# Performance work log

Measured on AMD Instinct MI355X. Metric: run time of the kernel, lower is better.

Reference implementation:

```python
import jax, jax.numpy as jnp
import numpy as np


def setup_inputs() -> dict:
    key = jax.random.key(0)
    kx, kq, kb, kc = jax.random.split(key, 4)
    N, D = 16384, 1024
    x = jax.random.normal(kx, (N, D), dtype=jnp.float32)
    Q = jax.random.normal(kq, (D, D), dtype=jnp.float32)
    b = jax.random.normal(kb, (D,), dtype=jnp.float32)
    c = jax.random.normal(kc, (1,), dtype=jnp.float32)
    return {"x": x, "Q": Q, "b": b, "c": c}


def reference(x, Q, b, c):
    # y_i = x_i^T Q x_i + b^T x_i + c  (same math as diag(x @ Q @ x.T)
    # without materializing the NxN matrix)
    xQ = x @ Q                                # [N, D]
    quad = jnp.sum(xQ * x, axis=-1)           # [N]
    y = quad + x @ b + c                       # [N] (c broadcasts from [1])
    return y[:, None]                          # [N, 1]
```

## Files before the change

### kernel.cpp

```cpp
#include <hip/hip_runtime.h>
#include <hip/hip_bf16.h>


#define DD 1024
#define KH 128
#define NPH 16
#define BUF_SHORTS 4096

typedef short v8s __attribute__((ext_vector_type(8)));
typedef float v4f __attribute__((ext_vector_type(4)));

#define AS1(p) ((const __attribute__((address_space(1))) void*)(p))
#define AS3(p) ((__attribute__((address_space(3))) void*)(p))

__device__ __forceinline__ short f2b(float f) {
    union { __hip_bfloat16 h; short s; } u;
    u.h = __float2bfloat16(f);
    return u.s;
}

__global__ __launch_bounds__(256)
void convert_q(const float* __restrict__ Q, short* __restrict__ qb)
{
    const int i = blockIdx.x * 256 + threadIdx.x;
    const float4 f = ((const float4*)Q)[i];
    short4 s;
    s.x = f2b(f.x); s.y = f2b(f.y); s.z = f2b(f.z); s.w = f2b(f.w);
    ((short4*)qb)[i] = s;
}

template<bool PRE>
__device__ __forceinline__
void quad_body(const float* __restrict__ x, const float* __restrict__ Qf,
               const short* __restrict__ Qb, const float* __restrict__ bvec,
               const float* __restrict__ cptr, float* __restrict__ y)
{
    __shared__ short lq[2][BUF_SHORTS];

    const int tid  = threadIdx.x;
    const int lane = tid & 63;
    const int quad = lane >> 4;
    const int l15  = lane & 15;
    const int wave = tid >> 6;

    const int seg  = blockIdx.x & 15;
    const int rblk = blockIdx.x >> 4;
    const int kq   = seg >> 1;
    const int cs   = seg & 1;

    const int row_base = rblk * 256 + wave * 64;
    const int kofs   = kq * KH;
    const int nbase0 = cs * 512;

    int srow[2], schunk[2];
    #pragma unroll
    for (int i = 0; i < 2; ++i) {
        const int slot = i * 256 + tid;
        const int r = slot >> 4, cp = slot & 15;
        srow[i] = r;
        schunk[i] = cp ^ (r & 7);
    }

    float4 pf[4];

    if (PRE) {
        #pragma unroll
        for (int i = 0; i < 2; ++i) {
            const short* src = Qb + (size_t)(nbase0 + srow[i]) * DD + kofs + schunk[i] * 8;
            __builtin_amdgcn_global_load_lds(AS1(src), AS3(&lq[0][(i * 256 + tid) * 8]), 16, 0, 0);
        }
    } else {
        #pragma unroll
        for (int i = 0; i < 2; ++i) {
            const float* src = Qf + (size_t)(nbase0 + srow[i]) * DD + kofs + schunk[i] * 8;
            pf[i * 2 + 0] = *(const float4*)(src);
            pf[i * 2 + 1] = *(const float4*)(src + 4);
        }
    }

    v8s a[4][4];
    #pragma unroll
    for (int g = 0; g < 4; ++g) {
        const float* xr = x + (size_t)(row_base + g * 16 + l15) * DD + kofs + quad * 8;
        #pragma unroll
        for (int s = 0; s < 4; ++s) {
            const float4 f0 = *(const float4*)(xr + s * 32);
            const float4 f1 = *(const float4*)(xr + s * 32 + 4);
            v8s t;
            t[0]=f2b(f0.x); t[1]=f2b(f0.y); t[2]=f2b(f0.z); t[3]=f2b(f0.w);
            t[4]=f2b(f1.x); t[5]=f2b(f1.y); t[6]=f2b(f1.z); t[7]=f2b(f1.w);
            a[g][s] = t;
            asm volatile("" : "+a"(a[g][s]));
        }
    }

    float acc[4][4];
    #pragma unroll
    for (int g = 0; g < 4; ++g)
        #pragma unroll
        for (int r = 0; r < 4; ++r) acc[g][r] = 0.f;

    for (int p = 0; p < NPH; ++p) {
        if (!PRE) {
            #pragma unroll
            for (int i = 0; i < 2; ++i) {
                const float4 f0 = pf[i * 2 + 0];
                const float4 f1 = pf[i * 2 + 1];
                v8s t;
                t[0]=f2b(f0.x); t[1]=f2b(f0.y); t[2]=f2b(f0.z); t[3]=f2b(f0.w);
                t[4]=f2b(f1.x); t[5]=f2b(f1.y); t[6]=f2b(f1.z); t[7]=f2b(f1.w);
                *(v8s*)&lq[p & 1][(i * 256 + tid) * 8] = t;
            }
        }
        __syncthreads();

        if (p + 1 < NPH) {
            const size_t base = (size_t)(nbase0 + (p + 1) * 32) * DD + kofs;
            if (PRE) {
                #pragma unroll
                for (int i = 0; i < 2; ++i) {
                    const short* src = Qb + base + (size_t)srow[i] * DD + schunk[i] * 8;
                    __builtin_amdgcn_global_load_lds(AS1(src),
                        AS3(&lq[(p + 1) & 1][(i * 256 + tid) * 8]), 16, 0, 0);
                }
            } else {
                #pragma unroll
                for (int i = 0; i < 2; ++i) {
                    const float* src = Qf + base + (size_t)srow[i] * DD + schunk[i] * 8;
                    pf[i * 2 + 0] = *(const float4*)(src);
                    pf[i * 2 + 1] = *(const float4*)(src + 4);
                }
            }
        }

        #pragma unroll
        for (int tau = 0; tau < 2; ++tau) {
            const int n = nbase0 + p * 32 + tau * 16 + l15;
            const float bn = (kq == 0) ? bvec[n] : 0.f;

            float xv[4][4];
            {
                const float* xc = x + (size_t)(row_base + quad * 4) * DD + n;
                #pragma unroll
                for (int g = 0; g < 4; ++g)
                    #pragma unroll
                    for (int r = 0; r < 4; ++r)
                        xv[g][r] = xc[(size_t)(g * 16 + r) * DD];
            }

            v4f cf[4];
            #pragma unroll
            for (int g = 0; g < 4; ++g) cf[g] = (v4f){0.f, 0.f, 0.f, 0.f};

            #pragma unroll
            for (int s = 0; s < 4; ++s) {
                const int phys = (quad + 4 * s) ^ (l15 & 7);
                const v8s bf = *(const v8s*)&lq[p & 1][((tau * 16 + l15) << 7) + (phys << 3)];
                #pragma unroll
                for (int g = 0; g < 4; ++g)
                    cf[g] = __builtin_amdgcn_mfma_f32_16x16x32_bf16(a[g][s], bf, cf[g], 0, 0, 0);
            }

            #pragma unroll
            for (int g = 0; g < 4; ++g)
                #pragma unroll
                for (int r = 0; r < 4; ++r)
                    acc[g][r] += (cf[g][r] + bn) * xv[g][r];
        }
    }

    const float cc = (seg == 0) ? cptr[0] : 0.f;
    #pragma unroll
    for (int g = 0; g < 4; ++g) {
        #pragma unroll
        for (int r = 0; r < 4; ++r) {
            float v = acc[g][r];
            v += __shfl_xor(v, 1); v += __shfl_xor(v, 2);
            v += __shfl_xor(v, 4); v += __shfl_xor(v, 8);
            if (l15 == 0)
                atomicAdd(&y[row_base + g * 16 + quad * 4 + r], v + cc);
        }
    }
}

__global__ __launch_bounds__(256, 3)
void quad_pre(const float* __restrict__ x, const short* __restrict__ Qb,
              const float* __restrict__ bvec, const float* __restrict__ cptr,
              float* __restrict__ y)
{
    quad_body<true>(x, nullptr, Qb, bvec, cptr, y);
}

__global__ __launch_bounds__(256, 2)
void quad_fp32(const float* __restrict__ x, const float* __restrict__ Qf,
               const float* __restrict__ bvec, const float* __restrict__ cptr,
               float* __restrict__ y)
{
    quad_body<false>(x, Qf, nullptr, bvec, cptr, y);
}

extern "C" void kernel_launch(void* const* d_in, const int* in_sizes, int n_in,
                              void* d_out, int out_size, void* d_ws, size_t ws_size,
                              hipStream_t stream)
{
    const float* x = (const float*)d_in[0];
    const float* Q = (const float*)d_in[1];
    const float* b = (const float*)d_in[2];
    const float* c = (const float*)d_in[3];
    float* y = (float*)d_out;

    hipMemsetAsync(y, 0, (size_t)out_size * sizeof(float), stream);

    if (ws_size >= (size_t)DD * DD * sizeof(short)) {
        short* qb = (short*)d_ws;
        convert_q<<<dim3(1024), dim3(256), 0, stream>>>(Q, qb);
        quad_pre<<<dim3(1024), dim3(256), 0, stream>>>(x, qb, b, c, y);
    } else {
        quad_fp32<<<dim3(1024), dim3(256), 0, stream>>>(x, Q, b, c, y);
    }
}
```

Baseline: 166.8 us.

## Double K-slice depth per block, widen Q phase tiles, prefetch x columns

Each block now covers a 256-wide K slice and loads 64 Q rows per phase, which halves the number of k-segments and the grid size. Fewer segments mean each x element is re-read by fewer blocks and fewer atomic partial sums reach y. The x-column and b values for the next 16-column tile are prefetched in registers while the current MFMAs run. In exchange, register use (a[4][8] held in AGPRs) and LDS per block (64 KB) both double, occupancy drops to 2 blocks per CU, and the grid shrinks to 512 blocks.

```diff
diff --git a/kernel.cpp b/kernel.cpp
--- a/kernel.cpp
+++ b/kernel.cpp
@@ -3,9 +3,11 @@
 
 
 #define DD 1024
-#define KH 128
-#define NPH 16
-#define BUF_SHORTS 4096
+#define KH 256
+#define KSTEP 8
+#define NPH 8
+#define ROW_SH 256
+#define BUF_SH (64 * ROW_SH)
 
 typedef short v8s __attribute__((ext_vector_type(8)));
 typedef float v4f __attribute__((ext_vector_type(4)));
@@ -35,55 +37,58 @@
                const short* __restrict__ Qb, const float* __restrict__ bvec,
                const float* __restrict__ cptr, float* __restrict__ y)
 {
-    __shared__ short lq[2][BUF_SHORTS];
+    __shared__ short lq[2][BUF_SH];
 
     const int tid  = threadIdx.x;
     const int lane = tid & 63;
+    const int wave = tid >> 6;
     const int quad = lane >> 4;
     const int l15  = lane & 15;
-    const int wave = tid >> 6;
-
-    const int seg  = blockIdx.x & 15;
-    const int rblk = blockIdx.x >> 4;
+
+    const int seg  = blockIdx.x & 7;
+    const int rblk = blockIdx.x >> 3;
     const int kq   = seg >> 1;
     const int cs   = seg & 1;
 
     const int row_base = rblk * 256 + wave * 64;
-    const int kofs   = kq * KH;
-    const int nbase0 = cs * 512;
-
-    int srow[2], schunk[2];
-    #pragma unroll
-    for (int i = 0; i < 2; ++i) {
+    const int kofs  = kq * KH;
+    const int nbase = cs * 512;
+
+    int srow[8], schunk[8];
+    #pragma unroll
+    for (int i = 0; i < 8; ++i) {
         const int slot = i * 256 + tid;
-        const int r = slot >> 4, cp = slot & 15;
+        const int r = slot >> 5, cp = slot & 31;
         srow[i] = r;
         schunk[i] = cp ^ (r & 7);
     }
 
-    float4 pf[4];
-
     if (PRE) {
         #pragma unroll
-        for (int i = 0; i < 2; ++i) {
-            const short* src = Qb + (size_t)(nbase0 + srow[i]) * DD + kofs + schunk[i] * 8;
-            __builtin_amdgcn_global_load_lds(AS1(src), AS3(&lq[0][(i * 256 + tid) * 8]), 16, 0, 0);
+        for (int i = 0; i < 8; ++i) {
+            const short* src = Qb + (size_t)(nbase + srow[i]) * DD + kofs + schunk[i] * 8;
+            __builtin_amdgcn_global_load_lds(AS1(src),
+                AS3(&lq[0][(i * 256 + tid) * 8]), 16, 0, 0);
         }
     } else {
         #pragma unroll
-        for (int i = 0; i < 2; ++i) {
-            const float* src = Qf + (size_t)(nbase0 + srow[i]) * DD + kofs + schunk[i] * 8;
-            pf[i * 2 + 0] = *(const float4*)(src);
-            pf[i * 2 + 1] = *(const float4*)(src + 4);
-        }
-    }
-
-    v8s a[4][4];
+        for (int i = 0; i < 8; ++i) {
+            const float* src = Qf + (size_t)(nbase + srow[i]) * DD + kofs + schunk[i] * 8;
+            const float4 f0 = *(const float4*)(src);
+            const float4 f1 = *(const float4*)(src + 4);
+            v8s t;
+            t[0]=f2b(f0.x); t[1]=f2b(f0.y); t[2]=f2b(f0.z); t[3]=f2b(f0.w);
+            t[4]=f2b(f1.x); t[5]=f2b(f1.y); t[6]=f2b(f1.z); t[7]=f2b(f1.w);
+            *(v8s*)&lq[0][(i * 256 + tid) * 8] = t;
+        }
+    }
+
+    v8s a[4][KSTEP];
     #pragma unroll
     for (int g = 0; g < 4; ++g) {
         const float* xr = x + (size_t)(row_base + g * 16 + l15) * DD + kofs + quad * 8;
         #pragma unroll
-        for (int s = 0; s < 4; ++s) {
+        for (int s = 0; s < KSTEP; ++s) {
             const float4 f0 = *(const float4*)(xr + s * 32);
             const float4 f1 = *(const float4*)(xr + s * 32 + 4);
             v8s t;
@@ -101,51 +106,58 @@
         for (int r = 0; r < 4; ++r) acc[g][r] = 0.f;
 
     for (int p = 0; p < NPH; ++p) {
-        if (!PRE) {
-            #pragma unroll
-            for (int i = 0; i < 2; ++i) {
-                const float4 f0 = pf[i * 2 + 0];
-                const float4 f1 = pf[i * 2 + 1];
-                v8s t;
-                t[0]=f2b(f0.x); t[1]=f2b(f0.y); t[2]=f2b(f0.z); t[3]=f2b(f0.w);
-                t[4]=f2b(f1.x); t[5]=f2b(f1.y); t[6]=f2b(f1.z); t[7]=f2b(f1.w);
-                *(v8s*)&lq[p & 1][(i * 256 + tid) * 8] = t;
-            }
-        }
         __syncthreads();
 
         if (p + 1 < NPH) {
-            const size_t base = (size_t)(nbase0 + (p + 1) * 32) * DD + kofs;
+            const size_t nb = (size_t)(nbase + (p + 1) * 64) * DD + kofs;
+            short* dst = &lq[(p + 1) & 1][0];
             if (PRE) {
                 #pragma unroll
-                for (int i = 0; i < 2; ++i) {
-                    const short* src = Qb + base + (size_t)srow[i] * DD + schunk[i] * 8;
+                for (int i = 0; i < 8; ++i) {
+                    const short* src = Qb + nb + (size_t)srow[i] * DD + schunk[i] * 8;
                     __builtin_amdgcn_global_load_lds(AS1(src),
-                        AS3(&lq[(p + 1) & 1][(i * 256 + tid) * 8]), 16, 0, 0);
+                        AS3(&dst[(i * 256 + tid) * 8]), 16, 0, 0);
                 }
             } else {
                 #pragma unroll
-                for (int i = 0; i < 2; ++i) {
-                    const float* src = Qf + base + (size_t)srow[i] * DD + schunk[i] * 8;
-                    pf[i * 2 + 0] = *(const float4*)(src);
-                    pf[i * 2 + 1] = *(const float4*)(src + 4);
+                for (int i = 0; i < 8; ++i) {
+                    const float* src = Qf + nb + (size_t)srow[i] * DD + schunk[i] * 8;
+                    const float4 f0 = *(const float4*)(src);
+                    const float4 f1 = *(const float4*)(src + 4);
+                    v8s t;
+                    t[0]=f2b(f0.x); t[1]=f2b(f0.y); t[2]=f2b(f0.z); t[3]=f2b(f0.w);
+                    t[4]=f2b(f1.x); t[5]=f2b(f1.y); t[6]=f2b(f1.z); t[7]=f2b(f1.w);
+                    *(v8s*)&dst[(i * 256 + tid) * 8] = t;
                 }
             }
         }
 
-        #pragma unroll
-        for (int tau = 0; tau < 2; ++tau) {
-            const int n = nbase0 + p * 32 + tau * 16 + l15;
-            const float bn = (kq == 0) ? bvec[n] : 0.f;
-
-            float xv[4][4];
-            {
+        const short* buf = &lq[p & 1][0];
+
+        float xva[4][4], xvb[4][4];
+        float bna, bnb;
+        {
+            const int n = nbase + p * 64 + l15;
+            bna = (kq == 0) ? bvec[n] : 0.f;
+            const float* xc = x + (size_t)(row_base + quad * 4) * DD + n;
+            #pragma unroll
+            for (int g = 0; g < 4; ++g)
+                #pragma unroll
+                for (int r = 0; r < 4; ++r)
+                    xva[g][r] = xc[(size_t)(g * 16 + r) * DD];
+        }
+
+        #pragma unroll
+        for (int tau = 0; tau < 4; ++tau) {
+            if (tau < 3) {
+                const int n = nbase + p * 64 + (tau + 1) * 16 + l15;
+                bnb = (kq == 0) ? bvec[n] : 0.f;
                 const float* xc = x + (size_t)(row_base + quad * 4) * DD + n;
                 #pragma unroll
                 for (int g = 0; g < 4; ++g)
                     #pragma unroll
                     for (int r = 0; r < 4; ++r)
-                        xv[g][r] = xc[(size_t)(g * 16 + r) * DD];
+                        xvb[g][r] = xc[(size_t)(g * 16 + r) * DD];
             }
 
             v4f cf[4];
@@ -153,9 +165,9 @@
             for (int g = 0; g < 4; ++g) cf[g] = (v4f){0.f, 0.f, 0.f, 0.f};
 
             #pragma unroll
-            for (int s = 0; s < 4; ++s) {
-                const int phys = (quad + 4 * s) ^ (l15 & 7);
-                const v8s bf = *(const v8s*)&lq[p & 1][((tau * 16 + l15) << 7) + (phys << 3)];
+            for (int s = 0; s < KSTEP; ++s) {
+                const int phys = (s * 4 + quad) ^ (l15 & 7);
+                const v8s bf = *(const v8s*)&buf[(tau * 16 + l15) * ROW_SH + phys * 8];
                 #pragma unroll
                 for (int g = 0; g < 4; ++g)
                     cf[g] = __builtin_amdgcn_mfma_f32_16x16x32_bf16(a[g][s], bf, cf[g], 0, 0, 0);
@@ -165,7 +177,13 @@
             for (int g = 0; g < 4; ++g)
                 #pragma unroll
                 for (int r = 0; r < 4; ++r)
-                    acc[g][r] += (cf[g][r] + bn) * xv[g][r];
+                    acc[g][r] += (cf[g][r] + bna) * xva[g][r];
+
+            bna = bnb;
+            #pragma unroll
+            for (int g = 0; g < 4; ++g)
+                #pragma unroll
+                for (int r = 0; r < 4; ++r) xva[g][r] = xvb[g][r];
         }
     }
 
@@ -183,7 +201,7 @@
     }
 }
 
-__global__ __launch_bounds__(256, 3)
+__global__ __launch_bounds__(256, 2)
 void quad_pre(const float* __restrict__ x, const short* __restrict__ Qb,
               const float* __restrict__ bvec, const float* __restrict__ cptr,
               float* __restrict__ y)
@@ -214,8 +232,8 @@
     if (ws_size >= (size_t)DD * DD * sizeof(short)) {
         short* qb = (short*)d_ws;
         convert_q<<<dim3(1024), dim3(256), 0, stream>>>(Q, qb);
-        quad_pre<<<dim3(1024), dim3(256), 0, stream>>>(x, qb, b, c, y);
+        quad_pre<<<dim3(512), dim3(256), 0, stream>>>(x, qb, b, c, y);
     } else {
-        quad_fp32<<<dim3(1024), dim3(256), 0, stream>>>(x, Q, b, c, y);
-    }
-}
+        quad_fp32<<<dim3(512), dim3(256), 0, stream>>>(x, Q, b, c, y);
+    }
+}
```

New measurement: 247.0 us. 1.48x slower.

## Restructure quadratic form as tiled 128x128 GEMM with fused epilogue reduction

Applied to the files above, without the earlier changes.

Replaces the split-K scheme, which kept x fragments in registers and gathered strided x columns inside the inner loop, with a standard 128x128 output-tile GEMM over the full K dimension. Both x and Q tiles are staged through double-buffered, swizzled LDS. The x·(xQ+b) dot product is applied only once in the epilogue, followed by a shuffle reduction and atomics. This removes the strided global gathers from the hot loop. In exchange, each x tile is reloaded and re-converted to bf16 once per column block (8x), and the loop synchronises every 32-wide K step.

```diff
diff --git a/kernel.cpp b/kernel.cpp
--- a/kernel.cpp
+++ b/kernel.cpp
@@ -3,9 +3,6 @@
 
 
 #define DD 1024
-#define KH 128
-#define NPH 16
-#define BUF_SHORTS 4096
 
 typedef short v8s __attribute__((ext_vector_type(8)));
 typedef float v4f __attribute__((ext_vector_type(4)));
@@ -19,166 +16,157 @@
     return u.s;
 }
 
+__device__ __forceinline__ v8s pack8(const float4& a, const float4& b) {
+    v8s t;
+    t[0]=f2b(a.x); t[1]=f2b(a.y); t[2]=f2b(a.z); t[3]=f2b(a.w);
+    t[4]=f2b(b.x); t[5]=f2b(b.y); t[6]=f2b(b.z); t[7]=f2b(b.w);
+    return t;
+}
+
 __global__ __launch_bounds__(256)
 void convert_q(const float* __restrict__ Q, short* __restrict__ qb)
 {
     const int i = blockIdx.x * 256 + threadIdx.x;
     const float4 f = ((const float4*)Q)[i];
     short4 s;
-    s.x = f2b(f.x); s.y = f2b(f.y); s.z = f2b(f.z); s.w = f2b(f.w);
+    s.x=f2b(f.x); s.y=f2b(f.y); s.z=f2b(f.z); s.w=f2b(f.w);
     ((short4*)qb)[i] = s;
 }
 
 template<bool PRE>
 __device__ __forceinline__
-void quad_body(const float* __restrict__ x, const float* __restrict__ Qf,
+void gemm_body(const float* __restrict__ x, const float* __restrict__ Qf,
                const short* __restrict__ Qb, const float* __restrict__ bvec,
                const float* __restrict__ cptr, float* __restrict__ y)
 {
-    __shared__ short lq[2][BUF_SHORTS];
+    __shared__ short lds[2][2][4096];
 
     const int tid  = threadIdx.x;
     const int lane = tid & 63;
+    const int wave = tid >> 6;
     const int quad = lane >> 4;
     const int l15  = lane & 15;
-    const int wave = tid >> 6;
-
-    const int seg  = blockIdx.x & 15;
-    const int rblk = blockIdx.x >> 4;
-    const int kq   = seg >> 1;
-    const int cs   = seg & 1;
-
-    const int row_base = rblk * 256 + wave * 64;
-    const int kofs   = kq * KH;
-    const int nbase0 = cs * 512;
-
-    int srow[2], schunk[2];
-    #pragma unroll
-    for (int i = 0; i < 2; ++i) {
-        const int slot = i * 256 + tid;
-        const int r = slot >> 4, cp = slot & 15;
-        srow[i] = r;
-        schunk[i] = cp ^ (r & 7);
-    }
-
-    float4 pf[4];
-
+    const int wr   = (wave >> 1) * 64;
+    const int wc   = (wave & 1) * 64;
+
+    const int mb = (int)blockIdx.x >> 3;
+    const int nb = (int)blockIdx.x & 7;
+    const int mbase = mb * 128;
+    const int nbase = nb * 128;
+
+    const int arow  = tid >> 1;
+    const int ahalf = tid & 1;
+    const float* xsrc = x + (size_t)(mbase + arow) * DD + ahalf * 16;
+    const int aslot0 = arow * 4 + ((ahalf * 2)     ^ (arow & 3));
+    const int aslot1 = arow * 4 + ((ahalf * 2 + 1) ^ (arow & 3));
+
+    const int bs0 = tid, bs1 = tid + 256;
+    const short* qsrc0 = PRE ? Qb + (size_t)(nbase + (bs0 >> 2)) * DD
+                                  + (((bs0 & 3) ^ ((bs0 >> 2) & 3)) * 8) : nullptr;
+    const short* qsrc1 = PRE ? Qb + (size_t)(nbase + (bs1 >> 2)) * DD
+                                  + (((bs1 & 3) ^ ((bs1 >> 2) & 3)) * 8) : nullptr;
+    const float* qfsrc = PRE ? nullptr
+                             : Qf + (size_t)(nbase + arow) * DD + ahalf * 16;
+
+    v4f acc[4][4];
+    #pragma unroll
+    for (int i = 0; i < 4; ++i)
+        #pragma unroll
+        for (int j = 0; j < 4; ++j) {
+            acc[i][j] = (v4f){0.f, 0.f, 0.f, 0.f};
+            asm volatile("" : "+a"(acc[i][j]));
+        }
+
+    float4 pfa[4], pfb[4];
+    #pragma unroll
+    for (int i = 0; i < 4; ++i) pfa[i] = *(const float4*)(xsrc + i * 4);
     if (PRE) {
-        #pragma unroll
-        for (int i = 0; i < 2; ++i) {
-            const short* src = Qb + (size_t)(nbase0 + srow[i]) * DD + kofs + schunk[i] * 8;
-            __builtin_amdgcn_global_load_lds(AS1(src), AS3(&lq[0][(i * 256 + tid) * 8]), 16, 0, 0);
-        }
+        __builtin_amdgcn_global_load_lds(AS1(qsrc0), AS3(&lds[0][1][bs0 * 8]), 16, 0, 0);
+        __builtin_amdgcn_global_load_lds(AS1(qsrc1), AS3(&lds[0][1][bs1 * 8]), 16, 0, 0);
     } else {
         #pragma unroll
-        for (int i = 0; i < 2; ++i) {
-            const float* src = Qf + (size_t)(nbase0 + srow[i]) * DD + kofs + schunk[i] * 8;
-            pf[i * 2 + 0] = *(const float4*)(src);
-            pf[i * 2 + 1] = *(const float4*)(src + 4);
-        }
-    }
-
-    v8s a[4][4];
-    #pragma unroll
-    for (int g = 0; g < 4; ++g) {
-        const float* xr = x + (size_t)(row_base + g * 16 + l15) * DD + kofs + quad * 8;
-        #pragma unroll
-        for (int s = 0; s < 4; ++s) {
-            const float4 f0 = *(const float4*)(xr + s * 32);
-            const float4 f1 = *(const float4*)(xr + s * 32 + 4);
-            v8s t;
-            t[0]=f2b(f0.x); t[1]=f2b(f0.y); t[2]=f2b(f0.z); t[3]=f2b(f0.w);
-            t[4]=f2b(f1.x); t[5]=f2b(f1.y); t[6]=f2b(f1.z); t[7]=f2b(f1.w);
-            a[g][s] = t;
-            asm volatile("" : "+a"(a[g][s]));
-        }
-    }
-
-    float acc[4][4];
-    #pragma unroll
-    for (int g = 0; g < 4; ++g)
-        #pragma unroll
-        for (int r = 0; r < 4; ++r) acc[g][r] = 0.f;
-
-    for (int p = 0; p < NPH; ++p) {
-        if (!PRE) {
-            #pragma unroll
-            for (int i = 0; i < 2; ++i) {
-                const float4 f0 = pf[i * 2 + 0];
-                const float4 f1 = pf[i * 2 + 1];
-                v8s t;
-                t[0]=f2b(f0.x); t[1]=f2b(f0.y); t[2]=f2b(f0.z); t[3]=f2b(f0.w);
-                t[4]=f2b(f1.x); t[5]=f2b(f1.y); t[6]=f2b(f1.z); t[7]=f2b(f1.w);
-                *(v8s*)&lq[p & 1][(i * 256 + tid) * 8] = t;
+        for (int i = 0; i < 4; ++i) pfb[i] = *(const float4*)(qfsrc + i * 4);
+        *(v8s*)&lds[0][1][aslot0 * 8] = pack8(pfb[0], pfb[1]);
+        *(v8s*)&lds[0][1][aslot1 * 8] = pack8(pfb[2], pfb[3]);
+    }
+    *(v8s*)&lds[0][0][aslot0 * 8] = pack8(pfa[0], pfa[1]);
+    *(v8s*)&lds[0][0][aslot1 * 8] = pack8(pfa[2], pfa[3]);
+
+    #pragma unroll
+    for (int i = 0; i < 4; ++i) pfa[i] = *(const float4*)(xsrc + 32 + i * 4);
+    if (!PRE) {
+        #pragma unroll
+        for (int i = 0; i < 4; ++i) pfb[i] = *(const float4*)(qfsrc + 32 + i * 4);
+    }
+
+    for (int it = 0; it < 32; ++it) {
+        __syncthreads();
+
+        const int cur = it & 1, nxt = cur ^ 1;
+        if (it + 1 < 32) {
+            const int kn = (it + 1) * 32;
+            if (PRE) {
+                __builtin_amdgcn_global_load_lds(AS1(qsrc0 + kn),
+                    AS3(&lds[nxt][1][bs0 * 8]), 16, 0, 0);
+                __builtin_amdgcn_global_load_lds(AS1(qsrc1 + kn),
+                    AS3(&lds[nxt][1][bs1 * 8]), 16, 0, 0);
+            } else {
+                *(v8s*)&lds[nxt][1][aslot0 * 8] = pack8(pfb[0], pfb[1]);
+                *(v8s*)&lds[nxt][1][aslot1 * 8] = pack8(pfb[2], pfb[3]);
             }
-        }
-        __syncthreads();
-
-        if (p + 1 < NPH) {
-            const size_t base = (size_t)(nbase0 + (p + 1) * 32) * DD + kofs;
-            if (PRE) {
+            *(v8s*)&lds[nxt][0][aslot0 * 8] = pack8(pfa[0], pfa[1]);
+            *(v8s*)&lds[nxt][0][aslot1 * 8] = pack8(pfa[2], pfa[3]);
+            if (it + 2 < 32) {
+                const int kn2 = (it + 2) * 32;
                 #pragma unroll
-                for (int i = 0; i < 2; ++i) {
-                    const short* src = Qb + base + (size_t)srow[i] * DD + schunk[i] * 8;
-                    __builtin_amdgcn_global_load_lds(AS1(src),
-                        AS3(&lq[(p + 1) & 1][(i * 256 + tid) * 8]), 16, 0, 0);
-                }
-            } else {
-                #pragma unroll
-                for (int i = 0; i < 2; ++i) {
-                    const float* src = Qf + base + (size_t)srow[i] * DD + schunk[i] * 8;
-                    pf[i * 2 + 0] = *(const float4*)(src);
-                    pf[i * 2 + 1] = *(const float4*)(src + 4);
+                for (int i = 0; i < 4; ++i)
+                    pfa[i] = *(const float4*)(xsrc + kn2 + i * 4);
+                if (!PRE) {
+                    #pragma unroll
+                    for (int i = 0; i < 4; ++i)
+                        pfb[i] = *(const float4*)(qfsrc + kn2 + i * 4);
                 }
             }
         }
 
-        #pragma unroll
-        for (int tau = 0; tau < 2; ++tau) {
-            const int n = nbase0 + p * 32 + tau * 16 + l15;
-            const float bn = (kq == 0) ? bvec[n] : 0.f;
-
-            float xv[4][4];
-            {
-                const float* xc = x + (size_t)(row_base + quad * 4) * DD + n;
-                #pragma unroll
-                for (int g = 0; g < 4; ++g)
-                    #pragma unroll
-                    for (int r = 0; r < 4; ++r)
-                        xv[g][r] = xc[(size_t)(g * 16 + r) * DD];
-            }
-
-            v4f cf[4];
+        const short* Ab = &lds[cur][0][0];
+        const short* Bb = &lds[cur][1][0];
+        v8s af[4], bf[4];
+        #pragma unroll
+        for (int i = 0; i < 4; ++i) {
+            const int rr = wr + i * 16 + l15;
+            af[i] = *(const v8s*)&Ab[(rr * 4 + (quad ^ (rr & 3))) * 8];
+        }
+        #pragma unroll
+        for (int j = 0; j < 4; ++j) {
+            const int rr = wc + j * 16 + l15;
+            bf[j] = *(const v8s*)&Bb[(rr * 4 + (quad ^ (rr & 3))) * 8];
+        }
+        #pragma unroll
+        for (int i = 0; i < 4; ++i)
             #pragma unroll
-            for (int g = 0; g < 4; ++g) cf[g] = (v4f){0.f, 0.f, 0.f, 0.f};
-
+            for (int j = 0; j < 4; ++j)
+                acc[i][j] = __builtin_amdgcn_mfma_f32_16x16x32_bf16(af[i], bf[j], acc[i][j], 0, 0, 0);
+    }
+
+    float bv[4];
+    #pragma unroll
+    for (int j = 0; j < 4; ++j) bv[j] = bvec[nbase + wc + j * 16 + l15];
+    const float cc = (nb == 0 && wc == 0) ? cptr[0] : 0.f;
+
+    #pragma unroll
+    for (int i = 0; i < 4; ++i) {
+        #pragma unroll
+        for (int r = 0; r < 4; ++r) {
+            const int m = mbase + wr + i * 16 + quad * 4 + r;
+            const float* xr = x + (size_t)m * DD + nbase + wc + l15;
+            float s = 0.f;
             #pragma unroll
-            for (int s = 0; s < 4; ++s) {
-                const int phys = (quad + 4 * s) ^ (l15 & 7);
-                const v8s bf = *(const v8s*)&lq[p & 1][((tau * 16 + l15) << 7) + (phys << 3)];
-                #pragma unroll
-                for (int g = 0; g < 4; ++g)
-                    cf[g] = __builtin_amdgcn_mfma_f32_16x16x32_bf16(a[g][s], bf, cf[g], 0, 0, 0);
-            }
-
-            #pragma unroll
-            for (int g = 0; g < 4; ++g)
-                #pragma unroll
-                for (int r = 0; r < 4; ++r)
-                    acc[g][r] += (cf[g][r] + bn) * xv[g][r];
-        }
-    }
-
-    const float cc = (seg == 0) ? cptr[0] : 0.f;
-    #pragma unroll
-    for (int g = 0; g < 4; ++g) {
-        #pragma unroll
-        for (int r = 0; r < 4; ++r) {
-            float v = acc[g][r];
-            v += __shfl_xor(v, 1); v += __shfl_xor(v, 2);
-            v += __shfl_xor(v, 4); v += __shfl_xor(v, 8);
-            if (l15 == 0)
-                atomicAdd(&y[row_base + g * 16 + quad * 4 + r], v + cc);
+            for (int j = 0; j < 4; ++j)
+                s += (acc[i][j][r] + bv[j]) * xr[j * 16];
+            s += __shfl_xor(s, 1); s += __shfl_xor(s, 2);
+            s += __shfl_xor(s, 4); s += __shfl_xor(s, 8);
+            if (l15 == 0) atomicAdd(&y[m], s + cc);
         }
     }
 }
@@ -188,7 +176,7 @@
               const float* __restrict__ bvec, const float* __restrict__ cptr,
               float* __restrict__ y)
 {
-    quad_body<true>(x, nullptr, Qb, bvec, cptr, y);
+    gemm_body<true>(x, nullptr, Qb, bvec, cptr, y);
 }
 
 __global__ __launch_bounds__(256, 2)
@@ -196,7 +184,7 @@
                const float* __restrict__ bvec, const float* __restrict__ cptr,
                float* __restrict__ y)
 {
-    quad_body<false>(x, Qf, nullptr, bvec, cptr, y);
+    gemm_body<false>(x, Qf, nullptr, bvec, cptr, y);
 }
 
 extern "C" void kernel_launch(void* const* d_in, const int* in_sizes, int n_in,
```

New measurement: 203.5 us. 22.0% more time.
